# Performance work log

Measured on AMD Instinct MI355X. Metric: run time of the kernel, lower is better.

The kernel has to match this reference:

```python
import jax, jax.numpy as jnp
import numpy as np

HID, INNER, CONV, L, DR = 1024, 2048, 4, 16, 64
B, S = 1, 2048


def setup_inputs() -> dict:
    key = jax.random.key(0)
    ks = jax.random.split(key, 8)
    def n(k, shape, scale=0.02):
        return jax.random.normal(k, shape, jnp.float32) * scale
    x = jax.random.normal(ks[0], (B, S, HID), jnp.float32)
    W_in = n(ks[1], (HID, 2 * INNER))                 # input_proj kernel (no bias)
    conv_w = n(ks[2], (CONV, 1, INNER), 0.1)          # depthwise conv kernel (W, I/g, O)
    conv_b = n(ks[3], (INNER,), 0.01)                 # conv bias
    W_x = n(ks[4], (INNER, DR + 2 * L))               # x_proj kernel (no bias)
    W_delta = n(ks[5], (DR, INNER), 0.05)             # delta_proj kernel
    b_delta = jnp.zeros((INNER,), jnp.float32)        # delta_proj bias
    A_log = jnp.log(jnp.tile(jnp.arange(1, L + 1, dtype=jnp.float32), (INNER, 1)))
    D = jnp.ones((INNER,), jnp.float32)
    W_out = n(ks[6], (INNER, HID))                    # out_proj kernel (no bias)
    return dict(x=x, W_in=W_in, conv_w=conv_w, conv_b=conv_b, W_x=W_x,
                W_delta=W_delta, b_delta=b_delta, A_log=A_log, D=D, W_out=W_out)


def _combine(left, right):
    # Associative op for linear recurrence h_t = a_t * h_{t-1} + b_t
    a1, b1 = left
    a2, b2 = right
    return a1 * a2, a2 * b1 + b2


def reference(x, W_in, conv_w, conv_b, W_x, W_delta, b_delta, A_log, D, W_out):
    b, s, _ = x.shape
    xz = x @ W_in                                     # [b,s,2*INNER]
    xi, z = xz[..., :INNER], xz[..., INNER:]
    # depthwise causal-ish conv: pad conv_dim-1 both sides (flax int padding), keep first s
    xc = jax.lax.conv_general_dilated(
        xi, conv_w, window_strides=(1,), padding=[(CONV - 1, CONV - 1)],
        dimension_numbers=('NWC', 'WIO', 'NWC'), feature_group_count=INNER)
    xc = jax.nn.silu(xc[:, :s, :] + conv_b)           # [b,s,INNER]
    # selective SSM
    A = -jnp.exp(A_log.astype(jnp.float32))           # [INNER,L]
    Df = D.astype(jnp.float32)
    xp = xc @ W_x                                     # [b,s,DR+2L]
    delta, Bm, Cm = xp[..., :DR], xp[..., DR:DR + L], xp[..., DR + L:]
    delta = jax.nn.softplus(delta @ W_delta + b_delta)  # [b,s,INNER]
    deltaA = jnp.exp(jnp.einsum('bsd,dl->bsdl', delta, A))            # [b,s,d,l]
    deltaBx = jnp.einsum('bsd,bsl,bsd->bsdl', delta, Bm, xc)          # [b,s,d,l]
    _, h = jax.lax.associative_scan(_combine, (deltaA, deltaBx), axis=1)
    y = jnp.einsum('bsdl,bsl->bsd', h, Cm) + xc * Df  # [b,s,INNER]
    y = y * jax.nn.silu(z)
    return y @ W_out                                  # [b,s,HID]
```

## Files before the change

kernel.cpp:

```cpp
#include <hip/hip_runtime.h>
#include <hip/hip_bf16.h>
#include <math.h>

#define S_LEN 2048
#define HID   1024
#define INNER 2048
#define NCONV 4
#define LSTATE 16
#define DRANK 64
#define XPW   96
#define CHUNK 32
#define NCHUNK (S_LEN / CHUNK)
#define XPAD  128
#define XPSPLIT 8

typedef __attribute__((ext_vector_type(8))) short bf16x8;
typedef __attribute__((ext_vector_type(4))) float f32x4;

__device__ __forceinline__ short f2bf(float f) {
  union { __hip_bfloat16 h; short s; } u;
  u.h = __float2bfloat16(f);
  return u.s;
}

__device__ __forceinline__ float fexp(float x) { return __expf(x); }

#define GLDS(gp, lp) __builtin_amdgcn_global_load_lds(                         \
    (const __attribute__((address_space(1))) unsigned int*)(gp),               \
    (__attribute__((address_space(3))) unsigned int*)(lp), 16, 0, 0)

#define NB_CAST (S_LEN * HID / 4 / 256)
#define NB_WIN  ((2 * INNER / 32) * (HID / 32))
#define NB_WOUT ((HID / 32) * (INNER / 32))
#define NB_WX   ((XPAD / 32) * (INNER / 32))
#define NB_PREP (NB_CAST + NB_WIN + NB_WOUT + NB_WX)
__global__ __launch_bounds__(256) void prep_kernel(
    const float* __restrict__ x, short* __restrict__ xb,
    const float* __restrict__ W_in, short* __restrict__ WinT,
    const float* __restrict__ W_out, short* __restrict__ WoutT,
    const float* __restrict__ W_x, short* __restrict__ WxT) {
  const int b = blockIdx.x;
  if (b < NB_CAST) {
    int i = b * 256 + threadIdx.x;
    const float4 v = ((const float4*)x)[i];
    short4 o;
    o.x = f2bf(v.x); o.y = f2bf(v.y); o.z = f2bf(v.z); o.w = f2bf(v.w);
    ((short4*)xb)[i] = o;
    return;
  }
  __shared__ float tile[32][33];
  const float* in; short* outp; int R, C, bx, by;
  if (b < NB_CAST + NB_WIN) {
    int bb = b - NB_CAST;
    in = W_in; outp = WinT; R = HID; C = 2 * INNER;
    bx = bb % (2 * INNER / 32); by = bb / (2 * INNER / 32);
  } else if (b < NB_CAST + NB_WIN + NB_WOUT) {
    int bb = b - NB_CAST - NB_WIN;
    in = W_out; outp = WoutT; R = INNER; C = HID;
    bx = bb % (HID / 32); by = bb / (HID / 32);
  } else {
    int bb = b - NB_CAST - NB_WIN - NB_WOUT;
    in = W_x; outp = WxT; R = INNER; C = XPW;
    bx = bb % (XPAD / 32); by = bb / (XPAD / 32);
  }
  const int bc = bx * 32, br = by * 32;
  const int tx = threadIdx.x & 31, ty = threadIdx.x >> 5;
  #pragma unroll
  for (int i = 0; i < 32; i += 8)
    tile[ty + i][tx] = (bc + tx < C)
        ? in[(size_t)(br + ty + i) * C + bc + tx] : 0.f;
  __syncthreads();
  #pragma unroll
  for (int i = 0; i < 32; i += 8)
    outp[(size_t)(bc + ty + i) * R + br + tx] = f2bf(tile[tx][ty + i]);
}

#define BK 32
__global__ __launch_bounds__(256) void gemm_bf16(
    const short* __restrict__ A,  int lda,
    const short* __restrict__ Bt, int ldb,
    float* __restrict__ C, int ldc,
    int kPerSplit, size_t cSliceStride) {
  __shared__ short As[3][128 * BK];
  __shared__ short Bs[3][128 * BK];
  const int tid  = threadIdx.x;
  const int lane = tid & 63;
  const int wave = tid >> 6;
  const int bm = blockIdx.y * 128;
  const int bn = blockIdx.x * 128;
  const int wm = (wave & 1) * 64;
  const int wn = (wave >> 1) * 64;
  const int fr = lane & 15;
  const int fq = lane >> 4;
  const int kbeg = blockIdx.z * kPerSplit;
  const int nIter = kPerSplit / BK;
  float* Cw = C + (size_t)blockIdx.z * cSliceStride;

  const int rs0 = wave * 32 + (lane >> 2);
  const int rs1 = rs0 + 16;
  const int sg0 = (lane & 3) ^ ((rs0 >> 1) & 3);
  const int sg1 = (lane & 3) ^ ((rs1 >> 1) & 3);
  const short* gA0 = A  + (size_t)(bm + rs0) * lda + kbeg + sg0 * 8;
  const short* gA1 = A  + (size_t)(bm + rs1) * lda + kbeg + sg1 * 8;
  const short* gB0 = Bt + (size_t)(bn + rs0) * ldb + kbeg + sg0 * 8;
  const short* gB1 = Bt + (size_t)(bn + rs1) * ldb + kbeg + sg1 * 8;
  const int ldsR0 = (wave * 32) * BK;
  const int ldsR1 = (wave * 32 + 16) * BK;

  f32x4 acc[4][4] = {};

  GLDS(gA0, &As[0][ldsR0]);
  GLDS(gA1, &As[0][ldsR1]);
  GLDS(gB0, &Bs[0][ldsR0]);
  GLDS(gB1, &Bs[0][ldsR1]);
  GLDS(gA0 + BK, &As[1][ldsR0]);
  GLDS(gA1 + BK, &As[1][ldsR1]);
  GLDS(gB0 + BK, &Bs[1][ldsR0]);
  GLDS(gB1 + BK, &Bs[1][ldsR1]);

  const int sl = (fq ^ ((fr >> 1) & 3)) * 8;
  for (int t = 0; t < nIter; ++t) {
    if (t + 1 < nIter) asm volatile("s_waitcnt vmcnt(4)" ::: "memory");
    else               asm volatile("s_waitcnt vmcnt(0)" ::: "memory");
    asm volatile("s_barrier" ::: "memory");
    if (t + 2 < nIter) {
      const int ko = (t + 2) * BK;
      const int w = (t + 2) % 3;
      GLDS(gA0 + ko, &As[w][ldsR0]);
      GLDS(gA1 + ko, &As[w][ldsR1]);
      GLDS(gB0 + ko, &Bs[w][ldsR0]);
      GLDS(gB1 + ko, &Bs[w][ldsR1]);
    }
    const int r = t % 3;
    bf16x8 af[4], bfv[4];
    #pragma unroll
    for (int mi = 0; mi < 4; ++mi)
      af[mi] = *(const bf16x8*)(&As[r][(wm + mi * 16 + fr) * BK + sl]);
    #pragma unroll
    for (int ni = 0; ni < 4; ++ni)
      bfv[ni] = *(const bf16x8*)(&Bs[r][(wn + ni * 16 + fr) * BK + sl]);
    #pragma unroll
    for (int mi = 0; mi < 4; ++mi)
      #pragma unroll
      for (int ni = 0; ni < 4; ++ni)
        acc[mi][ni] = __builtin_amdgcn_mfma_f32_16x16x32_bf16(
            af[mi], bfv[ni], acc[mi][ni], 0, 0, 0);
  }
  #pragma unroll
  for (int mi = 0; mi < 4; ++mi) {
    #pragma unroll
    for (int ni = 0; ni < 4; ++ni) {
      const int col = bn + wn + ni * 16 + fr;
      #pragma unroll
      for (int r = 0; r < 4; ++r) {
        const int row = bm + wm + mi * 16 + fq * 4 + r;
        Cw[(size_t)row * ldc + col] = acc[mi][ni][r];
      }
    }
  }
}

__global__ __launch_bounds__(256) void reduce_xp_kernel(
    const float* __restrict__ part, float* __restrict__ xp) {
  int i4 = blockIdx.x * 256 + threadIdx.x;
  if (i4 >= S_LEN * (XPW / 4)) return;
  int m = i4 / (XPW / 4);
  int n4 = i4 - m * (XPW / 4);
  const float4* p = (const float4*)part;
  const size_t rowv = (size_t)m * (XPAD / 4) + n4;
  const size_t slice = (size_t)S_LEN * (XPAD / 4);
  float4 o = p[rowv];
  #pragma unroll
  for (int s = 1; s < XPSPLIT; ++s) {
    float4 v = p[rowv + s * slice];
    o.x += v.x; o.y += v.y; o.z += v.z; o.w += v.w;
  }
  ((float4*)xp)[i4] = o;
}

__global__ __launch_bounds__(256) void reduce_out_kernel(
    const float* __restrict__ part, float* __restrict__ out) {
  int i4 = blockIdx.x * 256 + threadIdx.x;
  if (i4 >= S_LEN * (HID / 4)) return;
  const float4* p = (const float4*)part;
  const size_t slice = (size_t)S_LEN * (HID / 4);
  float4 a = p[i4], b = p[i4 + slice];
  float4 o;
  o.x = a.x + b.x; o.y = a.y + b.y; o.z = a.z + b.z; o.w = a.w + b.w;
  ((float4*)out)[i4] = o;
}

template<int EPI>
__global__ __launch_bounds__(256) void gemm_tiled(
    const float* __restrict__ A, int lda,
    const float* __restrict__ B, int ldb,
    float* __restrict__ C, int ldc,
    int M, int N, int K, const float* __restrict__ bias) {
  __shared__ float As[16][65];
  __shared__ float Bs[16][65];
  const int bm = blockIdx.y * 64;
  const int bn = blockIdx.x * 64;
  const int tid = threadIdx.x;
  const int tx = tid & 15;
  const int ty = tid >> 4;
  float acc[4][4] = {};
  for (int k0 = 0; k0 < K; k0 += 16) {
    #pragma unroll
    for (int i = tid; i < 64 * 16; i += 256) {
      int m = i >> 4, kk = i & 15;
      As[kk][m] = A[(size_t)(bm + m) * lda + k0 + kk];
    }
    #pragma unroll
    for (int i = tid; i < 16 * 64; i += 256) {
      int kk = i >> 6, n = i & 63;
      Bs[kk][n] = B[(size_t)(k0 + kk) * ldb + bn + n];
    }
    __syncthreads();
    #pragma unroll
    for (int kk = 0; kk < 16; ++kk) {
      float a[4], b[4];
      #pragma unroll
      for (int i = 0; i < 4; ++i) a[i] = As[kk][ty * 4 + i];
      #pragma unroll
      for (int j = 0; j < 4; ++j) b[j] = Bs[kk][tx * 4 + j];
      #pragma unroll
      for (int i = 0; i < 4; ++i)
        #pragma unroll
        for (int j = 0; j < 4; ++j)
          acc[i][j] += a[i] * b[j];
    }
    __syncthreads();
  }
  #pragma unroll
  for (int i = 0; i < 4; ++i) {
    #pragma unroll
    for (int j = 0; j < 4; ++j) {
      int row = bm + ty * 4 + i;
      int col = bn + tx * 4 + j;
      float v = acc[i][j];
      if (EPI == 1) {
        v += bias[col];
        v = fmaxf(v, 0.f) + log1pf(expf(-fabsf(v)));
      }
      C[(size_t)row * ldc + col] = v;
    }
  }
}

__global__ __launch_bounds__(256) void conv_silu_kernel(
    const float* __restrict__ xz,
    const float* __restrict__ cw,
    const float* __restrict__ cb,
    float* __restrict__ xc,
    short* __restrict__ xcb) {
  int i4 = blockIdx.x * 256 + threadIdx.x;
  if (i4 >= S_LEN * INNER / 4) return;
  int s = i4 / (INNER / 4);
  int cg = i4 - s * (INNER / 4);
  float4 acc = ((const float4*)cb)[cg];
  #pragma unroll
  for (int k = 0; k < NCONV; ++k) {
    int t = s - (NCONV - 1) + k;
    if (t >= 0) {
      float4 xv = *(const float4*)(xz + (size_t)t * (2 * INNER) + cg * 4);
      float4 wv = ((const float4*)(cw + k * INNER))[cg];
      acc.x += xv.x * wv.x; acc.y += xv.y * wv.y;
      acc.z += xv.z * wv.z; acc.w += xv.w * wv.w;
    }
  }
  float4 v;
  v.x = acc.x / (1.f + fexp(-acc.x));
  v.y = acc.y / (1.f + fexp(-acc.y));
  v.z = acc.z / (1.f + fexp(-acc.z));
  v.w = acc.w / (1.f + fexp(-acc.w));
  ((float4*)xc)[i4] = v;
  short4 o;
  o.x = f2bf(v.x); o.y = f2bf(v.y); o.z = f2bf(v.z); o.w = f2bf(v.w);
  ((short4*)xcb)[i4] = o;
}


__global__ __launch_bounds__(256) void scan_pass1(
    const float* __restrict__ delta,
    const float* __restrict__ xp,
    const float* __restrict__ xc,
    const float* __restrict__ A_log,
    float* __restrict__ Aprod,
    float* __restrict__ Hend) {
  __shared__ float Bc[CHUNK][LSTATE];
  const int tid = threadIdx.x;
  const int d = blockIdx.y * 256 + tid;
  const int c = blockIdx.x;
  const int s0 = c * CHUNK;
  for (int u = tid; u < CHUNK * LSTATE; u += 256) {
    int r = u >> 4, l = u & 15;
    Bc[r][l] = xp[(size_t)(s0 + r) * XPW + DRANK + l];
  }
  float a[LSTATE];
  {
    const float4* Ar = (const float4*)(A_log + (size_t)d * LSTATE);
    #pragma unroll
    for (int q = 0; q < 4; ++q) {
      float4 v = Ar[q];
      a[q * 4 + 0] = -fexp(v.x);
      a[q * 4 + 1] = -fexp(v.y);
      a[q * 4 + 2] = -fexp(v.z);
      a[q * 4 + 3] = -fexp(v.w);
    }
  }
  float h[LSTATE] = {}, ap[LSTATE];
  #pragma unroll
  for (int l = 0; l < LSTATE; ++l) ap[l] = 1.f;
  __syncthreads();
  const float* pd = delta + (size_t)s0 * INNER + d;
  const float* px = xc    + (size_t)s0 * INNER + d;
  for (int i = 0; i < CHUNK; ++i) {
    float dv = *pd, xcv = *px;
    pd += INNER; px += INNER;
    float sc = dv * xcv;
    #pragma unroll
    for (int l = 0; l < LSTATE; ++l) {
      float dA = fexp(dv * a[l]);
      h[l] = fmaf(dA, h[l], sc * Bc[i][l]);
      ap[l] *= dA;
    }
  }
  float4* Ap = (float4*)(Aprod + ((size_t)c * INNER + d) * LSTATE);
  float4* Hp = (float4*)(Hend  + ((size_t)c * INNER + d) * LSTATE);
  #pragma unroll
  for (int q = 0; q < 4; ++q) {
    Ap[q] = make_float4(ap[q * 4], ap[q * 4 + 1], ap[q * 4 + 2], ap[q * 4 + 3]);
    Hp[q] = make_float4(h[q * 4], h[q * 4 + 1], h[q * 4 + 2], h[q * 4 + 3]);
  }
}

__global__ __launch_bounds__(256) void scan_pass2(
    const float* __restrict__ Aprod, const float* __restrict__ Hend,
    float* __restrict__ Hin) {
  const int idx = blockIdx.x * 256 + threadIdx.x;
  const size_t stride = (size_t)INNER * LSTATE;
  float h = 0.f;
  for (int cb = 0; cb < NCHUNK; cb += 16) {
    float ap[16], he[16];
    #pragma unroll
    for (int j = 0; j < 16; ++j) {
      size_t o = (size_t)(cb + j) * stride + idx;
      ap[j] = Aprod[o];
      he[j] = Hend[o];
    }
    #pragma unroll
    for (int j = 0; j < 16; ++j) {
      size_t o = (size_t)(cb + j) * stride + idx;
      Hin[o] = h;
      h = ap[j] * h + he[j];
    }
  }
}

__global__ __launch_bounds__(256) void scan_pass3(
    const float* __restrict__ delta,
    const float* __restrict__ xp,
    const float* __restrict__ xc,
    const float* __restrict__ xz,
    const float* __restrict__ A_log,
    const float* __restrict__ Dvec,
    const float* __restrict__ Hin,
    short* __restrict__ ybf) {
  __shared__ float Bc[CHUNK][LSTATE];
  __shared__ float Cc[CHUNK][LSTATE];
  const int tid = threadIdx.x;
  const int d = blockIdx.y * 256 + tid;
  const int c = blockIdx.x;
  const int s0 = c * CHUNK;
  for (int u = tid; u < CHUNK * LSTATE; u += 256) {
    int r = u >> 4, l = u & 15;
    size_t base = (size_t)(s0 + r) * XPW + DRANK;
    Bc[r][l] = xp[base + l];
    Cc[r][l] = xp[base + LSTATE + l];
  }
  float a[LSTATE], h[LSTATE];
  {
    const float4* Ar = (const float4*)(A_log + (size_t)d * LSTATE);
    #pragma unroll
    for (int q = 0; q < 4; ++q) {
      float4 v = Ar[q];
      a[q * 4 + 0] = -fexp(v.x);
      a[q * 4 + 1] = -fexp(v.y);
      a[q * 4 + 2] = -fexp(v.z);
      a[q * 4 + 3] = -fexp(v.w);
    }
    const float4* Hi = (const float4*)(Hin + ((size_t)c * INNER + d) * LSTATE);
    #pragma unroll
    for (int q = 0; q < 4; ++q) {
      float4 v = Hi[q];
      h[q * 4 + 0] = v.x; h[q * 4 + 1] = v.y;
      h[q * 4 + 2] = v.z; h[q * 4 + 3] = v.w;
    }
  }
  const float Dd = Dvec[d];
  __syncthreads();
  const float* pd = delta + (size_t)s0 * INNER + d;
  const float* px = xc    + (size_t)s0 * INNER + d;
  const float* pz = xz + (size_t)s0 * (2 * INNER) + INNER + d;
  short* py = ybf + (size_t)s0 * INNER + d;
  for (int i = 0; i < CHUNK; ++i) {
    float dv = *pd, xcv = *px, zv = *pz;
    pd += INNER; px += INNER; pz += 2 * INNER;
    float sc = dv * xcv;
    float contrib = 0.f;
    #pragma unroll
    for (int l = 0; l < LSTATE; ++l) {
      float dA = fexp(dv * a[l]);
      h[l] = fmaf(dA, h[l], sc * Bc[i][l]);
      contrib = fmaf(h[l], Cc[i][l], contrib);
    }
    float silu_z = zv / (1.f + fexp(-zv));
    *py = f2bf(fmaf(xcv, Dd, contrib) * silu_z);
    py += INNER;
  }
}

extern "C" void kernel_launch(void* const* d_in, const int* in_sizes, int n_in,
                              void* d_out, int out_size, void* d_ws, size_t ws_size,
                              hipStream_t stream) {
  const float* x      = (const float*)d_in[0];
  const float* W_in   = (const float*)d_in[1];
  const float* conv_w = (const float*)d_in[2];
  const float* conv_b = (const float*)d_in[3];
  const float* W_x    = (const float*)d_in[4];
  const float* W_delta= (const float*)d_in[5];
  const float* b_delta= (const float*)d_in[6];
  const float* A_log  = (const float*)d_in[7];
  const float* Dvec   = (const float*)d_in[8];
  const float* W_out  = (const float*)d_in[9];
  float* out = (float*)d_out;

  float* ws    = (float*)d_ws;
  float* xz    = ws;
  float* xc    = xz + (size_t)S_LEN * 2 * INNER;
  float* xp    = xc + (size_t)S_LEN * INNER;
  float* delta = xp + (size_t)S_LEN * XPW;
  float* Aprod = delta + (size_t)S_LEN * INNER;
  float* Hend  = Aprod + (size_t)NCHUNK * INNER * LSTATE;
  float* Hin   = Hend  + (size_t)NCHUNK * INNER * LSTATE;
  short* xb    = (short*)(Hin + (size_t)NCHUNK * INNER * LSTATE);
  short* WinT  = xb + (size_t)S_LEN * HID;
  short* WoutT = WinT + (size_t)(2 * INNER) * HID;
  short* ybf   = WoutT + (size_t)HID * INNER;
  short* xcb   = ybf + (size_t)S_LEN * INNER;
  short* WxT   = xcb + (size_t)S_LEN * INNER;
  float* xpPart  = Aprod;
  float* outPart = Aprod;

  prep_kernel<<<NB_PREP, 256, 0, stream>>>(
      x, xb, W_in, WinT, W_out, WoutT, W_x, WxT);

  gemm_bf16<<<dim3(4096 / 128, 2048 / 128, 1), 256, 0, stream>>>(
      xb, HID, WinT, HID, xz, 2 * INNER, HID, 0);

  conv_silu_kernel<<<(S_LEN * INNER / 4 + 255) / 256, 256, 0, stream>>>(
      xz, conv_w, conv_b, xc, xcb);

  gemm_bf16<<<dim3(1, 2048 / 128, XPSPLIT), 256, 0, stream>>>(
      xcb, INNER, WxT, INNER, xpPart, XPAD, INNER / XPSPLIT,
      (size_t)S_LEN * XPAD);
  reduce_xp_kernel<<<(S_LEN * (XPW / 4) + 255) / 256, 256, 0, stream>>>(
      xpPart, xp);

  gemm_tiled<1><<<dim3(2048 / 64, 2048 / 64), 256, 0, stream>>>(
      xp, XPW, W_delta, INNER, delta, INNER, S_LEN, INNER, DRANK, b_delta);

  scan_pass1<<<dim3(NCHUNK, INNER / 256), 256, 0, stream>>>(
      delta, xp, xc, A_log, Aprod, Hend);
  scan_pass2<<<(INNER * LSTATE) / 256, 256, 0, stream>>>(Aprod, Hend, Hin);
  scan_pass3<<<dim3(NCHUNK, INNER / 256), 256, 0, stream>>>(
      delta, xp, xc, xz, A_log, Dvec, Hin, ybf);

  gemm_bf16<<<dim3(1024 / 128, 2048 / 128, 2), 256, 0, stream>>>(
      ybf, INNER, WoutT, INNER, outPart, HID, INNER / 2,
      (size_t)S_LEN * HID);
  reduce_out_kernel<<<(S_LEN * (HID / 4) + 255) / 256, 256, 0, stream>>>(
      outPart, out);
}
```

Baseline: 190.7 us.

## Move delta projection onto bf16 MFMA GEMM and widen GEMM to 512 threads

The fp32 tiled delta-projection GEMM with softplus epilogue is replaced by the bf16 MFMA GEMM, which gains a templated bias+softplus epilogue. W_delta is transposed to bf16 in prep, and the x_proj reduce also emits a bf16 copy of the delta columns. The MFMA GEMM now runs 512 threads (8 waves, each 64x32), where half the waves load A and half load B, with a 4-deep LDS ring buffer. Split-K is raised for x_proj (16) and out_proj (4), and out partials now reuse the xc buffer. This trades bf16 rounding on the delta path and extra reduction traffic for more parallelism and tensor-core use.

```diff
diff --git a/kernel.cpp b/kernel.cpp
--- a/kernel.cpp
+++ b/kernel.cpp
@@ -12,7 +12,8 @@
 #define CHUNK 32
 #define NCHUNK (S_LEN / CHUNK)
 #define XPAD  128
-#define XPSPLIT 8
+#define XPSPLIT 16
+#define OSPLIT  4
 
 typedef __attribute__((ext_vector_type(8))) short bf16x8;
 typedef __attribute__((ext_vector_type(4))) float f32x4;
@@ -33,12 +34,14 @@
 #define NB_WIN  ((2 * INNER / 32) * (HID / 32))
 #define NB_WOUT ((HID / 32) * (INNER / 32))
 #define NB_WX   ((XPAD / 32) * (INNER / 32))
-#define NB_PREP (NB_CAST + NB_WIN + NB_WOUT + NB_WX)
+#define NB_WD   ((INNER / 32) * (DRANK / 32))
+#define NB_PREP (NB_CAST + NB_WIN + NB_WOUT + NB_WX + NB_WD)
 __global__ __launch_bounds__(256) void prep_kernel(
     const float* __restrict__ x, short* __restrict__ xb,
     const float* __restrict__ W_in, short* __restrict__ WinT,
     const float* __restrict__ W_out, short* __restrict__ WoutT,
-    const float* __restrict__ W_x, short* __restrict__ WxT) {
+    const float* __restrict__ W_x, short* __restrict__ WxT,
+    const float* __restrict__ W_delta, short* __restrict__ WdT) {
   const int b = blockIdx.x;
   if (b < NB_CAST) {
     int i = b * 256 + threadIdx.x;
@@ -58,10 +61,14 @@
     int bb = b - NB_CAST - NB_WIN;
     in = W_out; outp = WoutT; R = INNER; C = HID;
     bx = bb % (HID / 32); by = bb / (HID / 32);
-  } else {
+  } else if (b < NB_CAST + NB_WIN + NB_WOUT + NB_WX) {
     int bb = b - NB_CAST - NB_WIN - NB_WOUT;
     in = W_x; outp = WxT; R = INNER; C = XPW;
     bx = bb % (XPAD / 32); by = bb / (XPAD / 32);
+  } else {
+    int bb = b - NB_CAST - NB_WIN - NB_WOUT - NB_WX;
+    in = W_delta; outp = WdT; R = DRANK; C = INNER;
+    bx = bb % (INNER / 32); by = bb / (INNER / 32);
   }
   const int bc = bx * 32, br = by * 32;
   const int tx = threadIdx.x & 31, ty = threadIdx.x >> 5;
@@ -75,93 +82,103 @@
     outp[(size_t)(bc + ty + i) * R + br + tx] = f2bf(tile[tx][ty + i]);
 }
 
-#define BK 32
-__global__ __launch_bounds__(256) void gemm_bf16(
+#define BK   32
+#define NBUF 4
+template<int EPI>
+__global__ __launch_bounds__(512) void gemm_bf16(
     const short* __restrict__ A,  int lda,
     const short* __restrict__ Bt, int ldb,
     float* __restrict__ C, int ldc,
-    int kPerSplit, size_t cSliceStride) {
-  __shared__ short As[3][128 * BK];
-  __shared__ short Bs[3][128 * BK];
+    int kPerSplit, size_t cSliceStride,
+    const float* __restrict__ bias) {
+  __shared__ short As[NBUF][128 * BK];
+  __shared__ short Bs[NBUF][128 * BK];
   const int tid  = threadIdx.x;
   const int lane = tid & 63;
   const int wave = tid >> 6;
   const int bm = blockIdx.y * 128;
   const int bn = blockIdx.x * 128;
   const int wm = (wave & 1) * 64;
-  const int wn = (wave >> 1) * 64;
+  const int wn = (wave >> 1) * 32;
   const int fr = lane & 15;
   const int fq = lane >> 4;
   const int kbeg = blockIdx.z * kPerSplit;
   const int nIter = kPerSplit / BK;
   float* Cw = C + (size_t)blockIdx.z * cSliceStride;
 
-  const int rs0 = wave * 32 + (lane >> 2);
+  const int sw  = wave & 3;
+  const int rs0 = sw * 32 + (lane >> 2);
   const int rs1 = rs0 + 16;
   const int sg0 = (lane & 3) ^ ((rs0 >> 1) & 3);
   const int sg1 = (lane & 3) ^ ((rs1 >> 1) & 3);
-  const short* gA0 = A  + (size_t)(bm + rs0) * lda + kbeg + sg0 * 8;
-  const short* gA1 = A  + (size_t)(bm + rs1) * lda + kbeg + sg1 * 8;
-  const short* gB0 = Bt + (size_t)(bn + rs0) * ldb + kbeg + sg0 * 8;
-  const short* gB1 = Bt + (size_t)(bn + rs1) * ldb + kbeg + sg1 * 8;
-  const int ldsR0 = (wave * 32) * BK;
-  const int ldsR1 = (wave * 32 + 16) * BK;
-
-  f32x4 acc[4][4] = {};
-
-  GLDS(gA0, &As[0][ldsR0]);
-  GLDS(gA1, &As[0][ldsR1]);
-  GLDS(gB0, &Bs[0][ldsR0]);
-  GLDS(gB1, &Bs[0][ldsR1]);
-  GLDS(gA0 + BK, &As[1][ldsR0]);
-  GLDS(gA1 + BK, &As[1][ldsR1]);
-  GLDS(gB0 + BK, &Bs[1][ldsR0]);
-  GLDS(gB1 + BK, &Bs[1][ldsR1]);
+  const bool isB = wave >= 4;
+  const short* gbase = isB ? Bt : A;
+  const int    gld   = isB ? ldb : lda;
+  const int    gro   = isB ? bn  : bm;
+  const short* g0 = gbase + (size_t)(gro + rs0) * gld + kbeg + sg0 * 8;
+  const short* g1 = gbase + (size_t)(gro + rs1) * gld + kbeg + sg1 * 8;
+  const int lo0 = (sw * 32) * BK;
+  const int lo1 = (sw * 32 + 16) * BK;
+
+  f32x4 acc[4][2] = {};
+
+#define STAGE(tile, buf) do {                                                  \
+    short* dst_ = isB ? &Bs[buf][0] : &As[buf][0];                             \
+    const int ko_ = (tile) * BK;                                               \
+    GLDS(g0 + ko_, dst_ + lo0);                                                \
+    GLDS(g1 + ko_, dst_ + lo1);                                                \
+  } while (0)
+
+  STAGE(0, 0);
+  if (nIter > 1) STAGE(1, 1);
+  if (nIter > 2) STAGE(2, 2);
 
   const int sl = (fq ^ ((fr >> 1) & 3)) * 8;
   for (int t = 0; t < nIter; ++t) {
-    if (t + 1 < nIter) asm volatile("s_waitcnt vmcnt(4)" ::: "memory");
+    const int rem = nIter - 1 - t;
+    if (rem >= 2)      asm volatile("s_waitcnt vmcnt(4)" ::: "memory");
+    else if (rem == 1) asm volatile("s_waitcnt vmcnt(2)" ::: "memory");
     else               asm volatile("s_waitcnt vmcnt(0)" ::: "memory");
     asm volatile("s_barrier" ::: "memory");
-    if (t + 2 < nIter) {
-      const int ko = (t + 2) * BK;
-      const int w = (t + 2) % 3;
-      GLDS(gA0 + ko, &As[w][ldsR0]);
-      GLDS(gA1 + ko, &As[w][ldsR1]);
-      GLDS(gB0 + ko, &Bs[w][ldsR0]);
-      GLDS(gB1 + ko, &Bs[w][ldsR1]);
-    }
-    const int r = t % 3;
-    bf16x8 af[4], bfv[4];
+    if (t + 3 < nIter) STAGE(t + 3, (t + 3) & 3);
+    const int r = t & 3;
+    bf16x8 af[4], bfv[2];
     #pragma unroll
     for (int mi = 0; mi < 4; ++mi)
       af[mi] = *(const bf16x8*)(&As[r][(wm + mi * 16 + fr) * BK + sl]);
     #pragma unroll
-    for (int ni = 0; ni < 4; ++ni)
+    for (int ni = 0; ni < 2; ++ni)
       bfv[ni] = *(const bf16x8*)(&Bs[r][(wn + ni * 16 + fr) * BK + sl]);
     #pragma unroll
     for (int mi = 0; mi < 4; ++mi)
       #pragma unroll
-      for (int ni = 0; ni < 4; ++ni)
+      for (int ni = 0; ni < 2; ++ni)
         acc[mi][ni] = __builtin_amdgcn_mfma_f32_16x16x32_bf16(
             af[mi], bfv[ni], acc[mi][ni], 0, 0, 0);
   }
+#undef STAGE
   #pragma unroll
   for (int mi = 0; mi < 4; ++mi) {
     #pragma unroll
-    for (int ni = 0; ni < 4; ++ni) {
+    for (int ni = 0; ni < 2; ++ni) {
       const int col = bn + wn + ni * 16 + fr;
       #pragma unroll
       for (int r = 0; r < 4; ++r) {
         const int row = bm + wm + mi * 16 + fq * 4 + r;
-        Cw[(size_t)row * ldc + col] = acc[mi][ni][r];
+        float v = acc[mi][ni][r];
+        if (EPI == 1) {
+          v += bias[col];
+          v = fmaxf(v, 0.f) + log1pf(expf(-fabsf(v)));
+        }
+        Cw[(size_t)row * ldc + col] = v;
       }
     }
   }
 }
 
 __global__ __launch_bounds__(256) void reduce_xp_kernel(
-    const float* __restrict__ part, float* __restrict__ xp) {
+    const float* __restrict__ part, float* __restrict__ xp,
+    short* __restrict__ xpb64) {
   int i4 = blockIdx.x * 256 + threadIdx.x;
   if (i4 >= S_LEN * (XPW / 4)) return;
   int m = i4 / (XPW / 4);
@@ -176,6 +193,11 @@
     o.x += v.x; o.y += v.y; o.z += v.z; o.w += v.w;
   }
   ((float4*)xp)[i4] = o;
+  if (n4 < DRANK / 4) {
+    short4 s4;
+    s4.x = f2bf(o.x); s4.y = f2bf(o.y); s4.z = f2bf(o.z); s4.w = f2bf(o.w);
+    ((short4*)xpb64)[m * (DRANK / 4) + n4] = s4;
+  }
 }
 
 __global__ __launch_bounds__(256) void reduce_out_kernel(
@@ -184,67 +206,13 @@
   if (i4 >= S_LEN * (HID / 4)) return;
   const float4* p = (const float4*)part;
   const size_t slice = (size_t)S_LEN * (HID / 4);
-  float4 a = p[i4], b = p[i4 + slice];
-  float4 o;
-  o.x = a.x + b.x; o.y = a.y + b.y; o.z = a.z + b.z; o.w = a.w + b.w;
+  float4 o = p[i4];
+  #pragma unroll
+  for (int s = 1; s < OSPLIT; ++s) {
+    float4 v = p[i4 + s * slice];
+    o.x += v.x; o.y += v.y; o.z += v.z; o.w += v.w;
+  }
   ((float4*)out)[i4] = o;
-}
-
-template<int EPI>
-__global__ __launch_bounds__(256) void gemm_tiled(
-    const float* __restrict__ A, int lda,
-    const float* __restrict__ B, int ldb,
-    float* __restrict__ C, int ldc,
-    int M, int N, int K, const float* __restrict__ bias) {
-  __shared__ float As[16][65];
-  __shared__ float Bs[16][65];
-  const int bm = blockIdx.y * 64;
-  const int bn = blockIdx.x * 64;
-  const int tid = threadIdx.x;
-  const int tx = tid & 15;
-  const int ty = tid >> 4;
-  float acc[4][4] = {};
-  for (int k0 = 0; k0 < K; k0 += 16) {
-    #pragma unroll
-    for (int i = tid; i < 64 * 16; i += 256) {
-      int m = i >> 4, kk = i & 15;
-      As[kk][m] = A[(size_t)(bm + m) * lda + k0 + kk];
-    }
-    #pragma unroll
-    for (int i = tid; i < 16 * 64; i += 256) {
-      int kk = i >> 6, n = i & 63;
-      Bs[kk][n] = B[(size_t)(k0 + kk) * ldb + bn + n];
-    }
-    __syncthreads();
-    #pragma unroll
-    for (int kk = 0; kk < 16; ++kk) {
-      float a[4], b[4];
-      #pragma unroll
-      for (int i = 0; i < 4; ++i) a[i] = As[kk][ty * 4 + i];
-      #pragma unroll
-      for (int j = 0; j < 4; ++j) b[j] = Bs[kk][tx * 4 + j];
-      #pragma unroll
-      for (int i = 0; i < 4; ++i)
-        #pragma unroll
-        for (int j = 0; j < 4; ++j)
-          acc[i][j] += a[i] * b[j];
-    }
-    __syncthreads();
-  }
-  #pragma unroll
-  for (int i = 0; i < 4; ++i) {
-    #pragma unroll
-    for (int j = 0; j < 4; ++j) {
-      int row = bm + ty * 4 + i;
-      int col = bn + tx * 4 + j;
-      float v = acc[i][j];
-      if (EPI == 1) {
-        v += bias[col];
-        v = fmaxf(v, 0.f) + log1pf(expf(-fabsf(v)));
-      }
-      C[(size_t)row * ldc + col] = v;
-    }
-  }
 }
 
 __global__ __launch_bounds__(256) void conv_silu_kernel(
@@ -449,26 +417,28 @@
   short* ybf   = WoutT + (size_t)HID * INNER;
   short* xcb   = ybf + (size_t)S_LEN * INNER;
   short* WxT   = xcb + (size_t)S_LEN * INNER;
+  short* WdT   = WxT + (size_t)XPAD * INNER;
+  short* xpb64 = WdT + (size_t)INNER * DRANK;
   float* xpPart  = Aprod;
-  float* outPart = Aprod;
+  float* outPart = xc;
 
   prep_kernel<<<NB_PREP, 256, 0, stream>>>(
-      x, xb, W_in, WinT, W_out, WoutT, W_x, WxT);
-
-  gemm_bf16<<<dim3(4096 / 128, 2048 / 128, 1), 256, 0, stream>>>(
-      xb, HID, WinT, HID, xz, 2 * INNER, HID, 0);
+      x, xb, W_in, WinT, W_out, WoutT, W_x, WxT, W_delta, WdT);
+
+  gemm_bf16<0><<<dim3(4096 / 128, 2048 / 128, 1), 512, 0, stream>>>(
+      xb, HID, WinT, HID, xz, 2 * INNER, HID, 0, nullptr);
 
   conv_silu_kernel<<<(S_LEN * INNER / 4 + 255) / 256, 256, 0, stream>>>(
       xz, conv_w, conv_b, xc, xcb);
 
-  gemm_bf16<<<dim3(1, 2048 / 128, XPSPLIT), 256, 0, stream>>>(
+  gemm_bf16<0><<<dim3(1, 2048 / 128, XPSPLIT), 512, 0, stream>>>(
       xcb, INNER, WxT, INNER, xpPart, XPAD, INNER / XPSPLIT,
-      (size_t)S_LEN * XPAD);
+      (size_t)S_LEN * XPAD, nullptr);
   reduce_xp_kernel<<<(S_LEN * (XPW / 4) + 255) / 256, 256, 0, stream>>>(
-      xpPart, xp);
-
-  gemm_tiled<1><<<dim3(2048 / 64, 2048 / 64), 256, 0, stream>>>(
-      xp, XPW, W_delta, INNER, delta, INNER, S_LEN, INNER, DRANK, b_delta);
+      xpPart, xp, xpb64);
+
+  gemm_bf16<1><<<dim3(2048 / 128, 2048 / 128, 1), 512, 0, stream>>>(
+      xpb64, DRANK, WdT, DRANK, delta, INNER, DRANK, 0, b_delta);
 
   scan_pass1<<<dim3(NCHUNK, INNER / 256), 256, 0, stream>>>(
       delta, xp, xc, A_log, Aprod, Hend);
@@ -476,9 +446,9 @@
   scan_pass3<<<dim3(NCHUNK, INNER / 256), 256, 0, stream>>>(
       delta, xp, xc, xz, A_log, Dvec, Hin, ybf);
 
-  gemm_bf16<<<dim3(1024 / 128, 2048 / 128, 2), 256, 0, stream>>>(
-      ybf, INNER, WoutT, INNER, outPart, HID, INNER / 2,
-      (size_t)S_LEN * HID);
+  gemm_bf16<0><<<dim3(1024 / 128, 2048 / 128, OSPLIT), 512, 0, stream>>>(
+      ybf, INNER, WoutT, INNER, outPart, HID, INNER / OSPLIT,
+      (size_t)S_LEN * HID, nullptr);
   reduce_out_kernel<<<(S_LEN * (HID / 4) + 255) / 256, 256, 0, stream>>>(
       outPart, out);
 }
```

Measured after the change: 169.8 us. -11.0%, faster.
